# Kernel optimization log

Hardware: AMD Instinct MI355X
Metric: run time of the kernel (lower is better)

The kernel has to match this reference:

```python
import jax, jax.numpy as jnp
import numpy as np

N = 100_000   # nodes
E = 3_200_000 # edges
K = 3         # num_stacks
T = 4         # num_layers (shared weights)
H = 16        # hidden channels of conv1
EPS = 1e-5    # BatchNorm eps


def setup_inputs() -> dict:
    key = jax.random.key(0)
    ks = jax.random.split(key, 12)
    def glorot(k, shape):
        fan = shape[-2] + shape[-1]
        return jax.random.normal(k, shape, jnp.float32) * (2.0 / fan) ** 0.5
    return {
        "x": jax.random.normal(ks[0], (N, 1), jnp.float32),
        "edge_index": jax.random.randint(ks[1], (2, E), 0, N, jnp.int32),
        "edge_weight": jax.random.uniform(ks[2], (E,), jnp.float32),
        # conv1: in=1, out=16  (init_weight [K,Fin,Fout], shared weight [K,Fout,Fout], root [K,Fin,Fout], bias [K,Fout])
        "conv1_init_w": glorot(ks[3], (K, 1, H)),
        "conv1_w": glorot(ks[4], (K, H, H)),
        "conv1_root_w": glorot(ks[5], (K, 1, H)),
        "conv1_bias": jnp.zeros((K, H), jnp.float32),
        # BatchNorm1d(16) in eval mode: running stats + affine params
        "bn1_gamma": jnp.ones((H,), jnp.float32),
        "bn1_beta": jnp.zeros((H,), jnp.float32),
        "bn1_mean": jnp.zeros((H,), jnp.float32),
        "bn1_var": jnp.ones((H,), jnp.float32),
        # conv2: in=16, out=1, act=None
        "conv2_init_w": glorot(ks[6], (K, H, 1)),
        "conv2_w": glorot(ks[7], (K, 1, 1)),
        "conv2_root_w": glorot(ks[8], (K, H, 1)),
        "conv2_bias": jnp.zeros((K, 1), jnp.float32),
    }


def _gcn_norm(edge_index, edge_weight):
    # ARMAConv uses gcn_norm with add_self_loops=False
    row, col = edge_index[0], edge_index[1]
    deg = jax.ops.segment_sum(edge_weight, col, num_segments=N)
    dis = jnp.where(deg > 0, jax.lax.rsqrt(jnp.maximum(deg, 1e-12)), 0.0)
    norm = dis[row] * edge_weight * dis[col]
    return row, col, norm


def _arma(x, row, col, norm, init_w, w, root_w, bias, act):
    # x: [N, Fin]; out per stack: [K, N, Fout]
    root = jnp.einsum('nf,kfo->kno', x, root_w) + bias[:, None, :]
    out = jnp.einsum('nf,kfo->kno', x, init_w)
    for t in range(T):
        if t > 0:
            out = jnp.einsum('kno,kop->knp', out, w)  # shared weight
        msg = out[:, row, :] * norm[None, :, None]     # [K, E, F] gather + scale
        out = jax.ops.segment_sum(msg.transpose(1, 0, 2), col, num_segments=N)  # [N, K, F]
        out = out.transpose(1, 0, 2) + root            # scatter-add + skip (root)
        if act:
            out = jax.nn.relu(out)
    return out.mean(axis=0)  # mean over stacks -> [N, Fout]


def reference(x, edge_index, edge_weight,
              conv1_init_w, conv1_w, conv1_root_w, conv1_bias,
              bn1_gamma, bn1_beta, bn1_mean, bn1_var,
              conv2_init_w, conv2_w, conv2_root_w, conv2_bias):
    row, col, norm = _gcn_norm(edge_index, edge_weight)
    h = _arma(x, row, col, norm, conv1_init_w, conv1_w, conv1_root_w, conv1_bias, act=True)
    # BatchNorm1d (eval) + ReLU; dropout is identity in eval
    h = (h - bn1_mean) * jax.lax.rsqrt(bn1_var + EPS) * bn1_gamma + bn1_beta
    h = jax.nn.relu(h)
    h = _arma(h, row, col, norm, conv2_init_w, conv2_w, conv2_root_w, conv2_bias, act=False)
    return jax.nn.sigmoid(h)  # [N, 1]
```

## Files before the change

kernel.cpp:

```cpp
#include <hip/hip_runtime.h>
#include <math.h>

#define NN 100000
#define NE 3200000
#define NBUCK 782
#define EPB 4096
#define NBLK 782
#define SB_Q 16
#define SCAP 4608
#define BN_EPS 1e-5f

static inline size_t alignup(size_t v) { return (v + 255) & ~size_t(255); }

__device__ inline unsigned short f2bf(float x) {
  unsigned u = __float_as_uint(x);
  u += 0x7FFF + ((u >> 16) & 1);
  return (unsigned short)(u >> 16);
}
__device__ inline float bf2f(unsigned short h) {
  return __uint_as_float((unsigned)h << 16);
}
__device__ inline float edgew(int e) {
  return __uint_as_float((unsigned)e & 0xFFFE0000u);
}

__global__ void k_hist(const int* __restrict__ col, int* __restrict__ cntm) {
  __shared__ int cnt[NBUCK];
  for (int i = threadIdx.x; i < NBUCK; i += 256) cnt[i] = 0;
  __syncthreads();
  int e0 = blockIdx.x * EPB;
  int nE = min(EPB, NE - e0);
  for (int i = threadIdx.x; i < nE; i += 256) atomicAdd(&cnt[col[e0 + i] >> 7], 1);
  __syncthreads();
  int* dst = cntm + (size_t)blockIdx.x * NBUCK;
  for (int i = threadIdx.x; i < NBUCK; i += 256) dst[i] = cnt[i];
}

__global__ void k_scanb(const int* __restrict__ cntm, int* __restrict__ basem,
                        int* __restrict__ btot) {
  __shared__ int s[NBLK][SB_Q + 1];
  int q0 = blockIdx.x * SB_Q;
  int nq = min(SB_Q, NBUCK - q0);
  int t = threadIdx.x;
  for (int idx = t; idx < NBLK * SB_Q; idx += 256) {
    int i = idx >> 4, j = idx & 15;
    s[i][j] = (j < nq) ? cntm[(size_t)i * NBUCK + q0 + j] : 0;
  }
  __syncthreads();
  int wave = t >> 6, lane = t & 63;
  for (int j = wave; j < SB_Q; j += 4) {
    int carry = 0;
    for (int c = 0; c < (NBLK + 63) / 64; ++c) {
      int i = c * 64 + lane;
      int v = (i < NBLK) ? s[i][j] : 0;
      int x = v;
      #pragma unroll
      for (int d = 1; d < 64; d <<= 1) {
        int tt = __shfl_up(x, d, 64);
        if (lane >= d) x += tt;
      }
      if (i < NBLK) s[i][j] = x - v + carry;
      carry += __shfl(x, 63, 64);
    }
    if (lane == 0 && j < nq) {
      btot[q0 + j] = carry;
      basem[(size_t)NBLK * NBUCK + q0 + j] = carry;
    }
  }
  __syncthreads();
  for (int idx = t; idx < NBLK * SB_Q; idx += 256) {
    int i = idx >> 4, j = idx & 15;
    if (j < nq) basem[(size_t)i * NBUCK + q0 + j] = s[i][j];
  }
}

__global__ void k_scanq(const int* __restrict__ btot, int* __restrict__ gbase) {
  __shared__ int s[NBUCK];
  __shared__ int c[256];
  const int NCH = (NBUCK + 3) / 4;
  int t = threadIdx.x;
  for (int i = t; i < NBUCK; i += 256) s[i] = btot[i];
  __syncthreads();
  if (t < NCH) {
    int b0 = 4 * t, sum = 0;
    #pragma unroll
    for (int j = 0; j < 4; ++j) if (b0 + j < NBUCK) sum += s[b0 + j];
    c[t] = sum;
  }
  __syncthreads();
  for (int d = 1; d < NCH; d <<= 1) {
    int v = (t < NCH && t >= d) ? c[t - d] : 0;
    __syncthreads();
    if (t < NCH) c[t] += v;
    __syncthreads();
  }
  if (t < NCH) {
    int b0 = 4 * t;
    int run = (t > 0) ? c[t - 1] : 0;
    #pragma unroll
    for (int j = 0; j < 4; ++j)
      if (b0 + j < NBUCK) { int v = s[b0 + j]; s[b0 + j] = run; run += v; }
  }
  __syncthreads();
  for (int i = t; i < NBUCK; i += 256) gbase[i] = s[i];
}

__global__ void k_scat(const int* __restrict__ row, const int* __restrict__ col,
                       const float* __restrict__ ew, const int* __restrict__ basem,
                       const int* __restrict__ gbase, int2* __restrict__ bin) {
  __shared__ int segB[NBUCK];
  __shared__ int cnt[NBUCK];
  __shared__ int csc[256];
  __shared__ int2 stage[EPB];
  __shared__ unsigned short qarr[EPB];
  int b = blockIdx.x, t = threadIdx.x;
  const int* rowA = basem + (size_t)b * NBUCK;
  const int* rowB = basem + (size_t)(b + 1) * NBUCK;
  for (int i = t; i < NBUCK; i += 256) {
    int a = rowA[i];
    segB[i] = gbase[i] + a;
    cnt[i] = rowB[i] - a;
  }
  __syncthreads();
  const int NCH = (NBUCK + 3) / 4;
  int q4 = 4 * t;
  if (t < NCH) {
    int sum = 0;
    #pragma unroll
    for (int j = 0; j < 4; ++j) if (q4 + j < NBUCK) sum += cnt[q4 + j];
    csc[t] = sum;
  }
  __syncthreads();
  for (int d = 1; d < NCH; d <<= 1) {
    int v = (t < NCH && t >= d) ? csc[t - d] : 0;
    __syncthreads();
    if (t < NCH) csc[t] += v;
    __syncthreads();
  }
  if (t < NCH) {
    int run = (t > 0) ? csc[t - 1] : 0;
    #pragma unroll
    for (int j = 0; j < 4; ++j)
      if (q4 + j < NBUCK) {
        int v = cnt[q4 + j];
        segB[q4 + j] -= run;
        cnt[q4 + j] = run;
        run += v;
      }
  }
  __syncthreads();
  int e0 = b * EPB;
  int nE = min(EPB, NE - e0);
  for (int i = t; i < nE; i += 256) {
    int e = e0 + i;
    int cc = col[e], q = cc >> 7;
    int p = atomicAdd(&cnt[q], 1);
    stage[p] = make_int2(row[e] | ((cc & 127) << 17), __float_as_int(ew[e]));
    qarr[p] = (unsigned short)q;
  }
  __syncthreads();
  for (int p = t; p < nE; p += 256) {
    int q = qarr[p];
    bin[segB[q] + p] = stage[p];
  }
}

__global__ void k_build(const int* __restrict__ gbase, const int* __restrict__ btot,
                        const int2* __restrict__ bin,
                        int* __restrict__ csr, float* __restrict__ dis,
                        int* __restrict__ nstart, int* __restrict__ ncnt,
                        int* __restrict__ perm) {
  __shared__ int2 stage[SCAP];
  __shared__ int cnt[128];
  __shared__ float degw[128];
  __shared__ int off[129];
  __shared__ int dh[129];
  int b = blockIdx.x;
  int gb0 = gbase[b];
  int nb = btot[b];
  const int2* gb = bin + gb0;
  for (int i = threadIdx.x; i < 128; i += 256) { cnt[i] = 0; degw[i] = 0.f; }
  for (int i = threadIdx.x; i < 129; i += 256) dh[i] = 0;
  __syncthreads();
  for (int i = threadIdx.x; i < nb; i += 256) {
    int2 v = gb[i];
    if (i < SCAP) stage[i] = v;
    int c = (v.x >> 17) & 127;
    atomicAdd(&cnt[c], 1);
    atomicAdd(&degw[c], __int_as_float(v.y));
  }
  __syncthreads();
  if (threadIdx.x == 0) {
    int s = 0;
    for (int c = 0; c < 128; ++c) { off[c] = s; s += cnt[c]; }
    off[128] = s;
  }
  __syncthreads();
  for (int c = threadIdx.x; c < 128; c += 256) {
    int n = b * 128 + c;
    if (n < NN) {
      nstart[n] = gb0 + off[c];
      ncnt[n] = cnt[c];
      float d = degw[c];
      dis[n] = (d > 0.f) ? rsqrtf(fmaxf(d, 1e-12f)) : 0.f;
      atomicAdd(&dh[min(cnt[c], 127) + 1], 1);
    }
  }
  __syncthreads();
  if (threadIdx.x == 0) {
    for (int d = 1; d < 129; ++d) dh[d] += dh[d - 1];
  }
  __syncthreads();
  for (int c = threadIdx.x; c < 128; c += 256) {
    int n = b * 128 + c;
    if (n < NN) {
      int r = atomicAdd(&dh[min(cnt[c], 127)], 1);
      perm[b * 128 + r] = n;
    }
  }
  __syncthreads();
  for (int i = threadIdx.x; i < 128; i += 256) cnt[i] = 0;
  __syncthreads();
  int* cb = csr + gb0;
  for (int i = threadIdx.x; i < nb; i += 256) {
    int2 v = (i < SCAP) ? stage[i] : gb[i];
    int c = (v.x >> 17) & 127;
    int pos = off[c] + atomicAdd(&cnt[c], 1);
    unsigned u = (unsigned)v.y;
    u += 0xFFFFu + ((u >> 17) & 1);
    cb[pos] = (v.x & 0x1FFFF) | (int)(u & 0xFFFE0000u);
  }
}

__global__ void k_init1(const float* __restrict__ x, const float* __restrict__ rw,
                        const float* __restrict__ bias, const float* __restrict__ dis,
                        unsigned short* __restrict__ root1, float* __restrict__ s) {
  int idx = blockIdx.x * 256 + threadIdx.x;
  if (idx >= NN * 16) return;
  int n = idx >> 4, f = idx & 15;
  float xv = x[n];
  if (f == 0) s[n] = dis[n] * xv;
  root1[n * 48 + f]      = f2bf(xv * rw[f]      + bias[f]);
  root1[n * 48 + 16 + f] = f2bf(xv * rw[16 + f] + bias[16 + f]);
  root1[n * 48 + 32 + f] = f2bf(xv * rw[32 + f] + bias[32 + f]);
}

__global__ void k_prop_first(const float* __restrict__ s,
                             const unsigned short* __restrict__ root,
                             ushort4* __restrict__ outp, const int* __restrict__ csr,
                             const int* __restrict__ nstart, const int* __restrict__ ncnt,
                             const float* __restrict__ dis, const float* __restrict__ w,
                             const float* __restrict__ iw, const int* __restrict__ perm) {
  __shared__ float ws[768];
  for (int i = threadIdx.x; i < 768; i += 256) ws[i] = w[i];
  __syncthreads();
  int f = threadIdx.x & 15;
  int gid = (blockIdx.x * 256 + threadIdx.x) >> 4;
  if (gid >= NN) return;
  int n = perm[gid];
  int e0 = nstart[n], cnt = ncnt[n];
  float g = 0.f;
  for (int i = f; i < cnt; i += 16) {
    int e = csr[e0 + i];
    g = fmaf(edgew(e), s[e & 0x1FFFF], g);
  }
  #pragma unroll
  for (int d = 8; d; d >>= 1) g += __shfl_xor(g, d, 16);
  float dn = dis[n];
  float dg = dn * g;
  float a0 = fmaxf(fmaf(dg, iw[f],      bf2f(root[n * 48 + f])),      0.f);
  float a1 = fmaxf(fmaf(dg, iw[16 + f], bf2f(root[n * 48 + 16 + f])), 0.f);
  float a2 = fmaxf(fmaf(dg, iw[32 + f], bf2f(root[n * 48 + 32 + f])), 0.f);
  float n0 = 0.f, n1 = 0.f, n2 = 0.f;
  #pragma unroll
  for (int f2 = 0; f2 < 16; ++f2) {
    float b0 = __shfl(a0, f2, 16);
    float b1 = __shfl(a1, f2, 16);
    float b2v = __shfl(a2, f2, 16);
    n0 = fmaf(b0, ws[f2 * 16 + f], n0);
    n1 = fmaf(b1, ws[256 + f2 * 16 + f], n1);
    n2 = fmaf(b2v, ws[512 + f2 * 16 + f], n2);
  }
  ushort4 pk;
  pk.x = f2bf(dn * n0); pk.y = f2bf(dn * n1); pk.z = f2bf(dn * n2); pk.w = 0;
  outp[(size_t)n * 16 + f] = pk;
}

template <bool APPLY_W>
__global__ void k_prop16(const ushort4* __restrict__ in,
                         const unsigned short* __restrict__ root,
                         ushort4* __restrict__ outp, const int* __restrict__ csr,
                         const int* __restrict__ nstart, const int* __restrict__ ncnt,
                         const float* __restrict__ dis, const float* __restrict__ w,
                         const float* __restrict__ bng, const float* __restrict__ bnb,
                         const float* __restrict__ bnm, const float* __restrict__ bnv,
                         const float* __restrict__ iw2, const float* __restrict__ rw2,
                         const float* __restrict__ b2,
                         float4* __restrict__ root2, ushort4* __restrict__ o2,
                         const int* __restrict__ perm) {
  __shared__ float ws[768];
  if (APPLY_W) {
    for (int i = threadIdx.x; i < 768; i += 256) ws[i] = w[i];
    __syncthreads();
  }
  int f = threadIdx.x & 15;
  int gid = (blockIdx.x * 256 + threadIdx.x) >> 4;
  if (gid >= NN) return;
  int n = perm[gid];
  int e0 = nstart[n], cnt = ncnt[n];
  float a0 = 0.f, a1 = 0.f, a2 = 0.f;
  int i = 0;
  for (; i + 8 <= cnt; i += 8) {
    int e[8];
    ushort4 v[8];
    #pragma unroll
    for (int j = 0; j < 8; ++j) e[j] = csr[e0 + i + j];
    #pragma unroll
    for (int j = 0; j < 8; ++j) v[j] = in[(size_t)(e[j] & 0x1FFFF) * 16 + f];
    #pragma unroll
    for (int j = 0; j < 8; ++j) {
      float we = edgew(e[j]);
      a0 = fmaf(we, bf2f(v[j].x), a0);
      a1 = fmaf(we, bf2f(v[j].y), a1);
      a2 = fmaf(we, bf2f(v[j].z), a2);
    }
  }
  for (; i + 4 <= cnt; i += 4) {
    int e[4];
    ushort4 v[4];
    #pragma unroll
    for (int j = 0; j < 4; ++j) e[j] = csr[e0 + i + j];
    #pragma unroll
    for (int j = 0; j < 4; ++j) v[j] = in[(size_t)(e[j] & 0x1FFFF) * 16 + f];
    #pragma unroll
    for (int j = 0; j < 4; ++j) {
      float we = edgew(e[j]);
      a0 = fmaf(we, bf2f(v[j].x), a0);
      a1 = fmaf(we, bf2f(v[j].y), a1);
      a2 = fmaf(we, bf2f(v[j].z), a2);
    }
  }
  for (; i < cnt; ++i) {
    int e = csr[e0 + i];
    float we = edgew(e);
    ushort4 v = in[(size_t)(e & 0x1FFFF) * 16 + f];
    a0 = fmaf(we, bf2f(v.x), a0);
    a1 = fmaf(we, bf2f(v.y), a1);
    a2 = fmaf(we, bf2f(v.z), a2);
  }
  float dn = dis[n];
  a0 = fmaxf(fmaf(dn, a0, bf2f(root[n * 48 + f])),      0.f);
  a1 = fmaxf(fmaf(dn, a1, bf2f(root[n * 48 + 16 + f])), 0.f);
  a2 = fmaxf(fmaf(dn, a2, bf2f(root[n * 48 + 32 + f])), 0.f);
  if (APPLY_W) {
    float n0 = 0.f, n1 = 0.f, n2 = 0.f;
    #pragma unroll
    for (int f2 = 0; f2 < 16; ++f2) {
      float b0 = __shfl(a0, f2, 16);
      float b1 = __shfl(a1, f2, 16);
      float b2v = __shfl(a2, f2, 16);
      n0 = fmaf(b0, ws[f2 * 16 + f], n0);
      n1 = fmaf(b1, ws[256 + f2 * 16 + f], n1);
      n2 = fmaf(b2v, ws[512 + f2 * 16 + f], n2);
    }
    ushort4 pk;
    pk.x = f2bf(dn * n0); pk.y = f2bf(dn * n1); pk.z = f2bf(dn * n2); pk.w = 0;
    outp[(size_t)n * 16 + f] = pk;
  } else {
    float mean = (a0 + a1 + a2) * (1.f / 3.f);
    float hv = fmaxf((mean - bnm[f]) * rsqrtf(bnv[f] + BN_EPS) * bng[f] + bnb[f], 0.f);
    float d0 = hv * iw2[f],      r0 = hv * rw2[f];
    float d1 = hv * iw2[16 + f], r1 = hv * rw2[16 + f];
    float d2 = hv * iw2[32 + f], r2 = hv * rw2[32 + f];
    #pragma unroll
    for (int d = 8; d; d >>= 1) {
      d0 += __shfl_xor(d0, d, 16); r0 += __shfl_xor(r0, d, 16);
      d1 += __shfl_xor(d1, d, 16); r1 += __shfl_xor(r1, d, 16);
      d2 += __shfl_xor(d2, d, 16); r2 += __shfl_xor(r2, d, 16);
    }
    if (f == 0) {
      float4 rt;
      rt.x = r0 + b2[0]; rt.y = r1 + b2[1]; rt.z = r2 + b2[2]; rt.w = 0.f;
      root2[n] = rt;
      ushort4 pk;
      pk.x = f2bf(dn * d0); pk.y = f2bf(dn * d1); pk.z = f2bf(dn * d2); pk.w = 0;
      o2[n] = pk;
    }
  }
}

template <bool LAST>
__global__ void k_prop1(const ushort4* __restrict__ in, const float4* __restrict__ root,
                        ushort4* __restrict__ outp, float* __restrict__ outf,
                        const int* __restrict__ csr,
                        const int* __restrict__ nstart, const int* __restrict__ ncnt,
                        const float* __restrict__ dis, const float* __restrict__ w2,
                        const int* __restrict__ perm) {
  int lane = threadIdx.x & 15;
  int gid = (blockIdx.x * 256 + threadIdx.x) >> 4;
  if (gid >= NN) return;
  int n = perm[gid];
  int e0 = nstart[n], cnt = ncnt[n];
  float a0 = 0.f, a1 = 0.f, a2 = 0.f;
  for (int i = lane; i < cnt; i += 16) {
    int e = csr[e0 + i];
    float we = edgew(e);
    ushort4 src = in[e & 0x1FFFF];
    a0 = fmaf(we, bf2f(src.x), a0);
    a1 = fmaf(we, bf2f(src.y), a1);
    a2 = fmaf(we, bf2f(src.z), a2);
  }
  #pragma unroll
  for (int d = 8; d; d >>= 1) {
    a0 += __shfl_xor(a0, d, 16);
    a1 += __shfl_xor(a1, d, 16);
    a2 += __shfl_xor(a2, d, 16);
  }
  if (lane == 0) {
    float dn = dis[n];
    float4 rt = root[n];
    if (LAST) {
      float s = fmaf(dn, a0, rt.x) + fmaf(dn, a1, rt.y) + fmaf(dn, a2, rt.z);
      s *= (1.f / 3.f);
      outf[n] = 1.f / (1.f + expf(-s));
    } else {
      ushort4 pk;
      pk.x = f2bf(dn * fmaf(dn, a0, rt.x) * w2[0]);
      pk.y = f2bf(dn * fmaf(dn, a1, rt.y) * w2[1]);
      pk.z = f2bf(dn * fmaf(dn, a2, rt.z) * w2[2]);
      pk.w = 0;
      outp[n] = pk;
    }
  }
}

extern "C" void kernel_launch(void* const* d_in, const int* in_sizes, int n_in,
                              void* d_out, int out_size, void* d_ws, size_t ws_size,
                              hipStream_t stream) {
  const float* x     = (const float*)d_in[0];
  const int*   ei    = (const int*)d_in[1];
  const float* ew    = (const float*)d_in[2];
  const float* c1_iw = (const float*)d_in[3];
  const float* c1_w  = (const float*)d_in[4];
  const float* c1_rw = (const float*)d_in[5];
  const float* c1_b  = (const float*)d_in[6];
  const float* bn_g  = (const float*)d_in[7];
  const float* bn_b  = (const float*)d_in[8];
  const float* bn_m  = (const float*)d_in[9];
  const float* bn_v  = (const float*)d_in[10];
  const float* c2_iw = (const float*)d_in[11];
  const float* c2_w  = (const float*)d_in[12];
  const float* c2_rw = (const float*)d_in[13];
  const float* c2_b  = (const float*)d_in[14];
  float* out = (float*)d_out;

  char* p = (char*)d_ws;
  auto take = [&](size_t bytes) -> char* { char* r = p; p += alignup(bytes); return r; };
  int*     cntm   = (int*)take((size_t)NBLK * NBUCK * 4);
  int*     basem  = (int*)take((size_t)(NBLK + 1) * NBUCK * 4);
  int*     btot   = (int*)take((size_t)NBUCK * 4);
  int*     gbase  = (int*)take((size_t)NBUCK * 4);
  int2*    bin    = (int2*)take((size_t)NE * 8);
  int*     csr    = (int*)take((size_t)NE * 4);
  float*   dis    = (float*)take((size_t)NN * 4);
  int*     nst    = (int*)take((size_t)NN * 4);
  int*     ncn    = (int*)take((size_t)NN * 4);
  int*     perm   = (int*)take((size_t)NN * 4);
  unsigned short* root1 = (unsigned short*)take((size_t)NN * 48 * 2);
  float*   sbuf   = (float*)take((size_t)NN * 4);
  ushort4* bufA   = (ushort4*)take((size_t)NN * 16 * 8);
  ushort4* bufB   = (ushort4*)take((size_t)NN * 16 * 8);
  float4*  root2  = (float4*)take((size_t)NN * 16);
  ushort4* o2A    = (ushort4*)take((size_t)NN * 8);
  ushort4* o2B    = (ushort4*)take((size_t)NN * 8);

  const int* row = ei;
  const int* col = ei + NE;

  const int gP = (NN * 16 + 255) / 256;
  const int gSB = (NBUCK + SB_Q - 1) / SB_Q;

  k_hist <<<NBLK, 256, 0, stream>>>(col, cntm);
  k_scanb<<<gSB, 256, 0, stream>>>(cntm, basem, btot);
  k_scanq<<<1, 256, 0, stream>>>(btot, gbase);
  k_scat <<<NBLK, 256, 0, stream>>>(row, col, ew, basem, gbase, bin);
  k_build<<<NBUCK, 256, 0, stream>>>(gbase, btot, bin, csr, dis, nst, ncn, perm);

  k_init1<<<gP, 256, 0, stream>>>(x, c1_rw, c1_b, dis, root1, sbuf);
  k_prop_first<<<gP, 256, 0, stream>>>(sbuf, root1, bufA, csr, nst, ncn, dis, c1_w, c1_iw, perm);
  k_prop16<true ><<<gP, 256, 0, stream>>>(bufA, root1, bufB, csr, nst, ncn, dis, c1_w,
      nullptr, nullptr, nullptr, nullptr, nullptr, nullptr, nullptr, nullptr, nullptr, perm);
  k_prop16<true ><<<gP, 256, 0, stream>>>(bufB, root1, bufA, csr, nst, ncn, dis, c1_w,
      nullptr, nullptr, nullptr, nullptr, nullptr, nullptr, nullptr, nullptr, nullptr, perm);
  k_prop16<false><<<gP, 256, 0, stream>>>(bufA, root1, nullptr, csr, nst, ncn, dis, nullptr,
      bn_g, bn_b, bn_m, bn_v, c2_iw, c2_rw, c2_b, root2, o2A, perm);

  k_prop1<false><<<gP, 256, 0, stream>>>(o2A, root2, o2B, nullptr, csr, nst, ncn, dis, c2_w, perm);
  k_prop1<false><<<gP, 256, 0, stream>>>(o2B, root2, o2A, nullptr, csr, nst, ncn, dis, c2_w, perm);
  k_prop1<false><<<gP, 256, 0, stream>>>(o2A, root2, o2B, nullptr, csr, nst, ncn, dis, c2_w, perm);
  k_prop1<true ><<<gP, 256, 0, stream>>>(o2B, root2, nullptr, out, csr, nst, ncn, dis, c2_w, perm);
}
```

Measured before the change: 443.3 us.

## Relabel nodes into degree-sorted order so propagation kernels index directly

Node data is now stored in the permuted, degree-sorted order. The CSR source indices are rewritten through an inverse permutation in a new relabel pass, and x is gathered through perm at init while the final output is scattered back through perm. Propagation kernels then drop the perm indirection, so per-node reads and writes become contiguous instead of scattered. The cost is an extra pass over all 3.2M edges plus an iperm gather, and the gather targets change locality depending on how the permutation reorders nodes.

```diff
diff --git a/kernel.cpp b/kernel.cpp
--- a/kernel.cpp
+++ b/kernel.cpp
@@ -169,7 +169,7 @@
                         const int2* __restrict__ bin,
                         int* __restrict__ csr, float* __restrict__ dis,
                         int* __restrict__ nstart, int* __restrict__ ncnt,
-                        int* __restrict__ perm) {
+                        int* __restrict__ perm, int* __restrict__ iperm) {
   __shared__ int2 stage[SCAP];
   __shared__ int cnt[128];
   __shared__ float degw[128];
@@ -198,13 +198,7 @@
   __syncthreads();
   for (int c = threadIdx.x; c < 128; c += 256) {
     int n = b * 128 + c;
-    if (n < NN) {
-      nstart[n] = gb0 + off[c];
-      ncnt[n] = cnt[c];
-      float d = degw[c];
-      dis[n] = (d > 0.f) ? rsqrtf(fmaxf(d, 1e-12f)) : 0.f;
-      atomicAdd(&dh[min(cnt[c], 127) + 1], 1);
-    }
+    if (n < NN) atomicAdd(&dh[min(cnt[c], 127) + 1], 1);
   }
   __syncthreads();
   if (threadIdx.x == 0) {
@@ -215,7 +209,13 @@
     int n = b * 128 + c;
     if (n < NN) {
       int r = atomicAdd(&dh[min(cnt[c], 127)], 1);
-      perm[b * 128 + r] = n;
+      int nw = b * 128 + r;
+      perm[nw] = n;
+      iperm[n] = nw;
+      nstart[nw] = gb0 + off[c];
+      ncnt[nw] = cnt[c];
+      float d = degw[c];
+      dis[nw] = (d > 0.f) ? rsqrtf(fmaxf(d, 1e-12f)) : 0.f;
     }
   }
   __syncthreads();
@@ -232,13 +232,22 @@
   }
 }
 
+__global__ void k_relab(int* __restrict__ csr, const int* __restrict__ iperm) {
+  int i = blockIdx.x * 256 + threadIdx.x;
+  if (i < NE) {
+    int e = csr[i];
+    csr[i] = (int)((unsigned)e & 0xFFFE0000u) | iperm[e & 0x1FFFF];
+  }
+}
+
 __global__ void k_init1(const float* __restrict__ x, const float* __restrict__ rw,
                         const float* __restrict__ bias, const float* __restrict__ dis,
+                        const int* __restrict__ perm,
                         unsigned short* __restrict__ root1, float* __restrict__ s) {
   int idx = blockIdx.x * 256 + threadIdx.x;
   if (idx >= NN * 16) return;
   int n = idx >> 4, f = idx & 15;
-  float xv = x[n];
+  float xv = x[perm[n]];
   if (f == 0) s[n] = dis[n] * xv;
   root1[n * 48 + f]      = f2bf(xv * rw[f]      + bias[f]);
   root1[n * 48 + 16 + f] = f2bf(xv * rw[16 + f] + bias[16 + f]);
@@ -250,14 +259,13 @@
                              ushort4* __restrict__ outp, const int* __restrict__ csr,
                              const int* __restrict__ nstart, const int* __restrict__ ncnt,
                              const float* __restrict__ dis, const float* __restrict__ w,
-                             const float* __restrict__ iw, const int* __restrict__ perm) {
+                             const float* __restrict__ iw) {
   __shared__ float ws[768];
   for (int i = threadIdx.x; i < 768; i += 256) ws[i] = w[i];
   __syncthreads();
   int f = threadIdx.x & 15;
-  int gid = (blockIdx.x * 256 + threadIdx.x) >> 4;
-  if (gid >= NN) return;
-  int n = perm[gid];
+  int n = (blockIdx.x * 256 + threadIdx.x) >> 4;
+  if (n >= NN) return;
   int e0 = nstart[n], cnt = ncnt[n];
   float g = 0.f;
   for (int i = f; i < cnt; i += 16) {
@@ -296,17 +304,15 @@
                          const float* __restrict__ bnm, const float* __restrict__ bnv,
                          const float* __restrict__ iw2, const float* __restrict__ rw2,
                          const float* __restrict__ b2,
-                         float4* __restrict__ root2, ushort4* __restrict__ o2,
-                         const int* __restrict__ perm) {
+                         float4* __restrict__ root2, ushort4* __restrict__ o2) {
   __shared__ float ws[768];
   if (APPLY_W) {
     for (int i = threadIdx.x; i < 768; i += 256) ws[i] = w[i];
     __syncthreads();
   }
   int f = threadIdx.x & 15;
-  int gid = (blockIdx.x * 256 + threadIdx.x) >> 4;
-  if (gid >= NN) return;
-  int n = perm[gid];
+  int n = (blockIdx.x * 256 + threadIdx.x) >> 4;
+  if (n >= NN) return;
   int e0 = nstart[n], cnt = ncnt[n];
   float a0 = 0.f, a1 = 0.f, a2 = 0.f;
   int i = 0;
@@ -397,9 +403,8 @@
                         const float* __restrict__ dis, const float* __restrict__ w2,
                         const int* __restrict__ perm) {
   int lane = threadIdx.x & 15;
-  int gid = (blockIdx.x * 256 + threadIdx.x) >> 4;
-  if (gid >= NN) return;
-  int n = perm[gid];
+  int n = (blockIdx.x * 256 + threadIdx.x) >> 4;
+  if (n >= NN) return;
   int e0 = nstart[n], cnt = ncnt[n];
   float a0 = 0.f, a1 = 0.f, a2 = 0.f;
   for (int i = lane; i < cnt; i += 16) {
@@ -422,7 +427,7 @@
     if (LAST) {
       float s = fmaf(dn, a0, rt.x) + fmaf(dn, a1, rt.y) + fmaf(dn, a2, rt.z);
       s *= (1.f / 3.f);
-      outf[n] = 1.f / (1.f + expf(-s));
+      outf[perm[n]] = 1.f / (1.f + expf(-s));
     } else {
       ushort4 pk;
       pk.x = f2bf(dn * fmaf(dn, a0, rt.x) * w2[0]);
@@ -466,6 +471,7 @@
   int*     nst    = (int*)take((size_t)NN * 4);
   int*     ncn    = (int*)take((size_t)NN * 4);
   int*     perm   = (int*)take((size_t)NN * 4);
+  int*     iperm  = (int*)take((size_t)NN * 4);
   unsigned short* root1 = (unsigned short*)take((size_t)NN * 48 * 2);
   float*   sbuf   = (float*)take((size_t)NN * 4);
   ushort4* bufA   = (ushort4*)take((size_t)NN * 16 * 8);
@@ -479,21 +485,23 @@
 
   const int gP = (NN * 16 + 255) / 256;
   const int gSB = (NBUCK + SB_Q - 1) / SB_Q;
+  const int gE = (NE + 255) / 256;
 
   k_hist <<<NBLK, 256, 0, stream>>>(col, cntm);
   k_scanb<<<gSB, 256, 0, stream>>>(cntm, basem, btot);
   k_scanq<<<1, 256, 0, stream>>>(btot, gbase);
   k_scat <<<NBLK, 256, 0, stream>>>(row, col, ew, basem, gbase, bin);
-  k_build<<<NBUCK, 256, 0, stream>>>(gbase, btot, bin, csr, dis, nst, ncn, perm);
-
-  k_init1<<<gP, 256, 0, stream>>>(x, c1_rw, c1_b, dis, root1, sbuf);
-  k_prop_first<<<gP, 256, 0, stream>>>(sbuf, root1, bufA, csr, nst, ncn, dis, c1_w, c1_iw, perm);
+  k_build<<<NBUCK, 256, 0, stream>>>(gbase, btot, bin, csr, dis, nst, ncn, perm, iperm);
+  k_relab<<<gE, 256, 0, stream>>>(csr, iperm);
+
+  k_init1<<<gP, 256, 0, stream>>>(x, c1_rw, c1_b, dis, perm, root1, sbuf);
+  k_prop_first<<<gP, 256, 0, stream>>>(sbuf, root1, bufA, csr, nst, ncn, dis, c1_w, c1_iw);
   k_prop16<true ><<<gP, 256, 0, stream>>>(bufA, root1, bufB, csr, nst, ncn, dis, c1_w,
-      nullptr, nullptr, nullptr, nullptr, nullptr, nullptr, nullptr, nullptr, nullptr, perm);
+      nullptr, nullptr, nullptr, nullptr, nullptr, nullptr, nullptr, nullptr, nullptr);
   k_prop16<true ><<<gP, 256, 0, stream>>>(bufB, root1, bufA, csr, nst, ncn, dis, c1_w,
-      nullptr, nullptr, nullptr, nullptr, nullptr, nullptr, nullptr, nullptr, nullptr, perm);
+      nullptr, nullptr, nullptr, nullptr, nullptr, nullptr, nullptr, nullptr, nullptr);
   k_prop16<false><<<gP, 256, 0, stream>>>(bufA, root1, nullptr, csr, nst, ncn, dis, nullptr,
-      bn_g, bn_b, bn_m, bn_v, c2_iw, c2_rw, c2_b, root2, o2A, perm);
+      bn_g, bn_b, bn_m, bn_v, c2_iw, c2_rw, c2_b, root2, o2A);
 
   k_prop1<false><<<gP, 256, 0, stream>>>(o2A, root2, o2B, nullptr, csr, nst, ncn, dis, c2_w, perm);
   k_prop1<false><<<gP, 256, 0, stream>>>(o2B, root2, o2A, nullptr, csr, nst, ncn, dis, c2_w, perm);
```

After: 442.2 us. Within noise of the previous version (-0.2%).
